# Kernel tuning notes

Measured on AMD Instinct MI355X. Metric: run time of the kernel, lower is better.

The kernel has to match this reference:

```python
import jax, jax.numpy as jnp
import numpy as np

B, N = 16, 4096

def _fps(xyz, npoint):
    # iterative farthest point sampling on one cloud [n,3] -> [npoint] int32
    n = xyz.shape[0]
    def body(carry, _):
        dist, far = carry
        d = jnp.sum((xyz - xyz[far]) ** 2, axis=-1)
        dist = jnp.minimum(dist, d)
        return (dist, jnp.argmax(dist).astype(jnp.int32)), far
    _, idx = jax.lax.scan(body, (jnp.full((n,), 1e10, jnp.float32), jnp.int32(0)), None, length=npoint)
    return idx

def _ball_query(radius, nsample, xyz, new_xyz):
    # xyz [n,3], new_xyz [S,3] -> [S,nsample] neighbor indices (first-in-index order, as in PointNet++)
    n = xyz.shape[0]
    sqr = jnp.sum((new_xyz[:, None, :] - xyz[None, :, :]) ** 2, axis=-1)  # [S,n]
    idx = jnp.where(sqr > radius * radius, n, jnp.arange(n, dtype=jnp.int32)[None, :])
    idx = jnp.sort(idx, axis=-1)[:, :nsample]
    return jnp.where(idx == n, idx[:, :1], idx)

def _gather(p, i):
    return jax.vmap(lambda pp, ii: pp[ii])(p, i)

def _mlp(x, layers):
    # shared MLP = 1x1 conv over grouped points; BN(eval) folded into (W,b)
    for W, b in layers:
        x = jax.nn.relu(jnp.einsum('bsnc,co->bsno', x, W) + b)
    return x

def _sa(xyz, feats, npoint, radius, nsample, layers):
    fps_idx = jax.vmap(lambda p: _fps(p, npoint))(xyz)            # [B,S]
    new_xyz = _gather(xyz, fps_idx)                                # [B,S,3]
    idx = jax.vmap(lambda p, q: _ball_query(radius, nsample, p, q))(xyz, new_xyz)  # [B,S,ns]
    x = _gather(xyz, idx) - new_xyz[:, :, None, :]                 # centered grouped xyz
    if feats is not None:
        x = jnp.concatenate([x, _gather(feats, idx)], axis=-1)
    x = _mlp(x, layers)
    return new_xyz, jnp.max(x, axis=2)

def _forward(points, w10, b10, w11, b11, w12, b12, w20, b20, w21, b21, w22, b22, w30, b30, w31, b31, w32, b32, lw1, lb1, lw2, lb2, fw1, fb1, fw2, fb2, pos_mean, pos_std, rot_mean, rot_std):
    l1x, l1f = _sa(points, None, 512, 0.2, 32, [(w10, b10), (w11, b11), (w12, b12)])
    l2x, l2f = _sa(l1x, l1f, 128, 0.4, 64, [(w20, b20), (w21, b21), (w22, b22)])
    # sa3: group_all
    x = jnp.concatenate([l2x, l2f], axis=-1)[:, None]              # [B,1,128,259]
    x = _mlp(x, [(w30, b30), (w31, b31), (w32, b32)])
    g = jnp.max(x, axis=2).reshape(points.shape[0], 1024)
    label = jax.nn.sigmoid(jax.nn.relu(g @ lw1 + lb1) @ lw2 + lb2)  # dropout = identity (eval)
    res = jax.nn.relu(g @ fw1 + fb1) @ fw2 + fb2
    pl = res[:, 0:3] * pos_std + pos_mean
    rl = res[:, 3:9] * rot_std + rot_mean
    pr = res[:, 9:12] * pos_std + pos_mean
    rr = res[:, 12:18] * rot_std + rot_mean
    return jnp.concatenate([label, pl, rl, pr, rr], axis=-1)       # [B,20]

def setup_inputs():
    ks = iter(jax.random.split(jax.random.key(0), 64))
    def w(shape, s=0.05):
        return jax.random.normal(next(ks), shape, jnp.float32) * s
    inp = {'points': jax.random.normal(next(ks), (B, N, 3), jnp.float32) * 0.5}
    dims = {'w10': (3, 64), 'w11': (64, 64), 'w12': (64, 128), 'w20': (131, 128), 'w21': (128, 128), 'w22': (128, 256), 'w30': (259, 256), 'w31': (256, 512), 'w32': (512, 1024), 'lw1': (1024, 256), 'lw2': (256, 2), 'fw1': (1024, 512), 'fw2': (512, 18)}
    for name, s in dims.items():
        inp[name] = w(s)
        inp[name.replace('w', 'b', 1)] = jnp.zeros((s[1],), jnp.float32)
    inp['pos_mean'] = w((3,), 0.1)
    inp['pos_std'] = jnp.abs(w((3,))) + 1.0
    inp['rot_mean'] = w((6,), 0.1)
    inp['rot_std'] = jnp.abs(w((6,))) + 1.0
    return inp

def reference(points, w10, b10, w11, b11, w12, b12, w20, b20, w21, b21, w22, b22, w30, b30, w31, b31, w32, b32, lw1, lb1, lw2, lb2, fw1, fb1, fw2, fb2, pos_mean, pos_std, rot_mean, rot_std):
    return _forward(points, w10, b10, w11, b11, w12, b12, w20, b20, w21, b21, w22, b22, w30, b30, w31, b31, w32, b32, lw1, lb1, lw2, lb2, fw1, fb1, fw2, fb2, pos_mean, pos_std, rot_mean, rot_std)
```

## Files before the change

kernel.cpp:

```cpp
#include <hip/hip_runtime.h>
#include <math.h>

#define BB 16
#define NN 4096

typedef float v2f __attribute__((ext_vector_type(2)));
typedef short bfrag8 __attribute__((ext_vector_type(8)));
typedef float fx4 __attribute__((ext_vector_type(4)));

__device__ __forceinline__ v2f pkfma(v2f a, v2f b, v2f c) {
    return __builtin_elementwise_fma(a, b, c);
}

__device__ __forceinline__ fx4 mfma16(bfrag8 a, bfrag8 b, fx4 c) {
    return __builtin_amdgcn_mfma_f32_16x16x32_bf16(a, b, c, 0, 0, 0);
}

__device__ __forceinline__ unsigned short bf16rne(float v) {
    unsigned u = __float_as_uint(v);
    return (unsigned short)((u + 0x7FFFu + ((u >> 16) & 1u)) >> 16);
}
__device__ __forceinline__ void bf16split(float v, unsigned short& h, unsigned short& l) {
    h = bf16rne(v);
    float fh = __uint_as_float((unsigned)h << 16);
    l = bf16rne(v - fh);
}

__device__ __forceinline__ float sq3(float dx, float dy, float dz) {
    return __fadd_rn(__fadd_rn(__fmul_rn(dx, dx), __fmul_rn(dy, dy)), __fmul_rn(dz, dz));
}

template<int CTRL, int RMASK>
__device__ __forceinline__ unsigned long long dpp_max_step(unsigned long long P) {
    int lo = __builtin_amdgcn_update_dpp(0, (int)(unsigned)P,        CTRL, RMASK, 0xf, true);
    int hi = __builtin_amdgcn_update_dpp(0, (int)(unsigned)(P >> 32), CTRL, RMASK, 0xf, true);
    unsigned long long o = ((unsigned long long)(unsigned)hi << 32) | (unsigned)lo;
    return (o > P) ? o : P;
}

__device__ __forceinline__ unsigned long long dpp_wave_max_u64(unsigned long long P) {
    P = dpp_max_step<0x111, 0xf>(P);
    P = dpp_max_step<0x112, 0xf>(P);
    P = dpp_max_step<0x114, 0xf>(P);
    P = dpp_max_step<0x118, 0xf>(P);
    P = dpp_max_step<0x142, 0xa>(P);
    P = dpp_max_step<0x143, 0xc>(P);
    return P;
}

__device__ __forceinline__ unsigned long long u64max(unsigned long long a, unsigned long long b) {
    return (a > b) ? a : b;
}

template<int NPTS, int NPOINT, int TPB>
__global__ __launch_bounds__(TPB) void fps_kernel(const float* __restrict__ xyz,
                                                  float* __restrict__ newxyz,
                                                  float* __restrict__ out_t,
                                                  int ts) {
    constexpr int PPT = NPTS / TPB;
    constexpr int NW  = TPB / 64;
    static_assert(NPOINT <= TPB, "far-history latch needs NPOINT <= TPB");
    __shared__ float sx[NPTS], sy[NPTS], sz[NPTS];
    __shared__ __align__(16) unsigned long long slot[2][NW];
    const int b = blockIdx.x;
    const int tid = threadIdx.x;
    const float* base = xyz + (size_t)b * NPTS * 3;
    for (int i = tid; i < NPTS; i += TPB) {
        sx[i] = base[i * 3 + 0];
        sy[i] = base[i * 3 + 1];
        sz[i] = base[i * 3 + 2];
    }
    __syncthreads();
    float px[PPT], py[PPT], pz[PPT], dist[PPT];
#pragma unroll
    for (int k = 0; k < PPT; k++) {
        int p = tid + k * TPB;
        px[k] = sx[p]; py[k] = sy[p]; pz[k] = sz[p];
        dist[k] = 1e10f;
    }
    int far = 0;
    int myfar = 0;
    const int lane = tid & 63, wid = tid >> 6;
    for (int it = 0; it < NPOINT; it++) {
        if (tid == it) myfar = far;
        float fx = sx[far], fy = sy[far], fz = sz[far];
        float bv = -1.0f; int bi = 0;
#pragma unroll
        for (int k = 0; k < PPT; k++) {
            float d = sq3(px[k] - fx, py[k] - fy, pz[k] - fz);
            float nd = fminf(dist[k], d);
            dist[k] = nd;
            if (nd > bv) { bv = nd; bi = tid + k * TPB; }
        }
        unsigned long long P = ((unsigned long long)__float_as_uint(bv) << 32)
                             | (unsigned long long)(~(unsigned)bi & 0xFFFFFFFFull);
        P = dpp_wave_max_u64(P);
        int bufi = it & 1;
        if (lane == 63) slot[bufi][wid] = P;
        __syncthreads();
        unsigned long long v[NW];
#pragma unroll
        for (int w = 0; w < NW; w++) v[w] = slot[bufi][w];
#pragma unroll
        for (int st = NW / 2; st >= 1; st >>= 1)
#pragma unroll
            for (int w = 0; w < st; w++) v[w] = u64max(v[w], v[w + st]);
        far = (int)(~(unsigned)(v[0] & 0xFFFFFFFFull));
    }
    if (tid < NPOINT) {
        float fx = sx[myfar], fy = sy[myfar], fz = sz[myfar];
        newxyz[((size_t)b * NPOINT + tid) * 3 + 0] = fx;
        newxyz[((size_t)b * NPOINT + tid) * 3 + 1] = fy;
        newxyz[((size_t)b * NPOINT + tid) * 3 + 2] = fz;
        if (out_t) {
            out_t[0 * ts + b * NPOINT + tid] = fx;
            out_t[1 * ts + b * NPOINT + tid] = fy;
            out_t[2 * ts + b * NPOINT + tid] = fz;
        }
    }
}

template<int NS>
__device__ __forceinline__ void bq_body(const float* __restrict__ pts, int n,
                                        const float* __restrict__ centers, int S,
                                        float r2, int* __restrict__ outidx,
                                        int wave, int lane) {
    int b = wave / S, s = wave % S;
    const float* c = centers + ((size_t)b * S + s) * 3;
    float cx = c[0], cy = c[1], cz = c[2];
    const float* pb = pts + (size_t)b * n * 3;
    int* out = outidx + ((size_t)b * S + s) * NS;
    int total = 0, first = -1;
    int rounds = n >> 6;
    for (int r = 0; r < rounds; r++) {
        int p = (r << 6) + lane;
        float dx = pb[p * 3 + 0] - cx, dy = pb[p * 3 + 1] - cy, dz = pb[p * 3 + 2] - cz;
        float d = sq3(dx, dy, dz);
        bool pred = (d <= r2);
        unsigned long long mask = __ballot(pred);
        if (first < 0 && mask) first = (r << 6) + (__ffsll(mask) - 1);
        if (pred) {
            int rank = total + __popcll(mask & ((1ull << lane) - 1ull));
            if (rank < NS) out[rank] = p;
        }
        total += __popcll(mask);
        if (total >= NS) break;
    }
    for (int j = total + lane; j < NS; j += 64) out[j] = first;
}

__device__ __forceinline__ void wconv_one(const float* __restrict__ W, float* __restrict__ OF,
                                          int NT, int KT, int N, int t) {
    int L = t & 63;
    int rest = t >> 6;
    int nt = rest & (NT - 1);
    int hk = rest / NT;
    int kt = hk % KT, hl = hk / KT;
    int k0 = kt * 32 + (L >> 4) * 8;
    int n  = nt * 16 + (L & 15);
    unsigned o[4];
#pragma unroll
    for (int e = 0; e < 4; e++) {
        float va = W[(size_t)(k0 + 2 * e + 0) * N + n];
        float vb = W[(size_t)(k0 + 2 * e + 1) * N + n];
        unsigned short ha, la, hb, lb;
        bf16split(va, ha, la);
        bf16split(vb, hb, lb);
        o[e] = hl ? ((unsigned)la | ((unsigned)lb << 16))
                  : ((unsigned)ha | ((unsigned)hb << 16));
    }
    ((uint4*)OF)[t] = make_uint4(o[0], o[1], o[2], o[3]);
}

__global__ __launch_bounds__(512) void bq1_fps2_kernel(const float* __restrict__ points,
                                                       const float* __restrict__ l1x,
                                                       float* __restrict__ l2x,
                                                       float* __restrict__ x3t,
                                                       int* __restrict__ idx1,
                                                       float r2a,
                                                       const float* __restrict__ w21,
                                                       const float* __restrict__ w22,
                                                       const float* __restrict__ w11s,
                                                       const float* __restrict__ w12s,
                                                       const float* __restrict__ w20s,
                                                       float* __restrict__ w21f,
                                                       float* __restrict__ w22f,
                                                       float* __restrict__ w11f,
                                                       float* __restrict__ w12f,
                                                       float* __restrict__ w20f) {
    __shared__ float sx[512], sy[512], sz[512];
    const int tid = threadIdx.x;
    const int lane = tid & 63, wid = tid >> 6;
    if (blockIdx.x < 16) {
        if (wid != 0) return;
        const int b = blockIdx.x;
        const float* base = l1x + (size_t)b * 512 * 3;
        for (int i = lane; i < 512; i += 64) {
            sx[i] = base[i * 3 + 0];
            sy[i] = base[i * 3 + 1];
            sz[i] = base[i * 3 + 2];
        }
        float px[8], py[8], pz[8], dist[8];
#pragma unroll
        for (int k = 0; k < 8; k++) {
            int p = lane + k * 64;
            px[k] = sx[p]; py[k] = sy[p]; pz[k] = sz[p];
            dist[k] = 1e10f;
        }
        int far = 0, myfar0 = 0, myfar1 = 0;
        for (int it = 0; it < 128; it++) {
            if (lane == it) myfar0 = far;
            if (lane == it - 64) myfar1 = far;
            float fx = sx[far], fy = sy[far], fz = sz[far];
            float bv = -1.0f; int bi = 0;
#pragma unroll
            for (int k = 0; k < 8; k++) {
                float d = sq3(px[k] - fx, py[k] - fy, pz[k] - fz);
                float nd = fminf(dist[k], d);
                dist[k] = nd;
                if (nd > bv) { bv = nd; bi = lane + k * 64; }
            }
            unsigned long long P = ((unsigned long long)__float_as_uint(bv) << 32)
                                 | (unsigned long long)(~(unsigned)bi & 0xFFFFFFFFull);
            P = dpp_wave_max_u64(P);
            unsigned lo = (unsigned)__builtin_amdgcn_readlane((int)(unsigned)P, 63);
            far = (int)(~lo);
        }
        {
            int s0 = lane, s1 = lane + 64;
            float a = sx[myfar0], c1 = sy[myfar0], c2 = sz[myfar0];
            l2x[((size_t)b * 128 + s0) * 3 + 0] = a;
            l2x[((size_t)b * 128 + s0) * 3 + 1] = c1;
            l2x[((size_t)b * 128 + s0) * 3 + 2] = c2;
            x3t[0 * 2048 + b * 128 + s0] = a;
            x3t[1 * 2048 + b * 128 + s0] = c1;
            x3t[2 * 2048 + b * 128 + s0] = c2;
            float d = sx[myfar1], e = sy[myfar1], f = sz[myfar1];
            l2x[((size_t)b * 128 + s1) * 3 + 0] = d;
            l2x[((size_t)b * 128 + s1) * 3 + 1] = e;
            l2x[((size_t)b * 128 + s1) * 3 + 2] = f;
            x3t[0 * 2048 + b * 128 + s1] = d;
            x3t[1 * 2048 + b * 128 + s1] = e;
            x3t[2 * 2048 + b * 128 + s1] = f;
        }
    } else if (blockIdx.x < 1040) {
        int wave = (blockIdx.x - 16) * 8 + wid;
        bq_body<32>(points, 4096, l1x, 512, r2a, idx1, wave, lane);
    } else {
        int gt = (blockIdx.x - 1040) * 512 + tid;
        if (gt < 4096)       wconv_one(w21,        w21f, 8,  4, 128, gt);
        else if (gt < 12288) wconv_one(w22,        w22f, 16, 4, 256, gt - 4096);
        else if (gt < 13312) wconv_one(w11s,       w11f, 4,  2, 64,  gt - 12288);
        else if (gt < 15360) wconv_one(w12s,       w12f, 8,  2, 128, gt - 13312);
        else                 wconv_one(w20s + 384, w20f, 8,  4, 128, gt - 15360);
    }
}

__global__ __launch_bounds__(64, 2) void sa1_bq2_kernel(const float* __restrict__ xyz, const float* __restrict__ l1x,
                                                 const int* __restrict__ idx1,
                                                 const float* __restrict__ l2x, int* __restrict__ idx2, float r2b,
                                                 const float* __restrict__ W1, const float* __restrict__ B1,
                                                 const float* __restrict__ W2f, const float* __restrict__ B2,
                                                 const float* __restrict__ W3f, const float* __restrict__ B3,
                                                 float* __restrict__ l1f) {
    __shared__ short hsh[64 * 72];
    __shared__ short hsl[64 * 72];
    int lane = threadIdx.x;
    if (blockIdx.x < 2048) {
        bq_body<64>(l1x, 512, l2x, 128, r2b, idx2, blockIdx.x, lane);
        return;
    }
    int blk = blockIdx.x - 2048;
    int b = blk >> 8;
    int ct = lane >> 5, nn = lane & 31;
    int s = ((blk & 255) << 1) | ct;
    int center = b * 512 + s;
    int c0 = b * 512 + ((blk & 255) << 1);
    int ii = idx1[center * 32 + nn];
    float px = xyz[((size_t)b * NN + ii) * 3 + 0] - l1x[(size_t)center * 3 + 0];
    float py = xyz[((size_t)b * NN + ii) * 3 + 1] - l1x[(size_t)center * 3 + 1];
    float pz = xyz[((size_t)b * NN + ii) * 3 + 2] - l1x[(size_t)center * 3 + 2];
#pragma unroll
    for (int c2 = 0; c2 < 32; c2++) {
        int ca = 2 * c2, cb = 2 * c2 + 1;
        float v0 = fmaxf(B1[ca] + px * W1[ca] + py * W1[64 + ca] + pz * W1[128 + ca], 0.0f);
        float v1 = fmaxf(B1[cb] + px * W1[cb] + py * W1[64 + cb] + pz * W1[128 + cb], 0.0f);
        unsigned short h0, l0, h1, l1;
        bf16split(v0, h0, l0);
        bf16split(v1, h1, l1);
        int base = lane * 72 + ca;
        *(unsigned*)(&hsh[base]) = (unsigned)h0 | ((unsigned)h1 << 16);
        *(unsigned*)(&hsl[base]) = (unsigned)l0 | ((unsigned)l1 << 16);
    }
    __syncthreads();
    {
        fx4 acc[4][4];
#pragma unroll
        for (int mt = 0; mt < 4; mt++)
#pragma unroll
            for (int nt = 0; nt < 4; nt++) {
                float bn = B2[nt * 16 + (lane & 15)];
                acc[mt][nt] = (fx4){bn, bn, bn, bn};
// ... 45 lines not shown
#pragma unroll
        for (int mt = 0; mt < 4; mt++)
#pragma unroll
            for (int nt = 0; nt < 4; nt++) {
                float bn = B3[(nbase + nt) * 16 + (lane & 15)];
                acc[mt][nt] = (fx4){bn, bn, bn, bn};
            }
#pragma unroll
        for (int kt = 0; kt < 2; kt++) {
            bfrag8 ah[4], al[4];
#pragma unroll
            for (int mt = 0; mt < 4; mt++) {
                int idx = (mt * 16 + (lane & 15)) * 72 + kt * 32 + (lane >> 4) * 8;
                ah[mt] = *(const bfrag8*)(&hsh[idx]);
                al[mt] = *(const bfrag8*)(&hsl[idx]);
            }
#pragma unroll
            for (int nt = 0; nt < 4; nt++) {
                bfrag8 bh = w3v[(size_t)((0 + kt) * 8 + nbase + nt) * 64 + lane];
                bfrag8 bl = w3v[(size_t)((2 + kt) * 8 + nbase + nt) * 64 + lane];
#pragma unroll
                for (int mt = 0; mt < 4; mt++) {
                    acc[mt][nt] = mfma16(ah[mt], bh, acc[mt][nt]);
                    acc[mt][nt] = mfma16(ah[mt], bl, acc[mt][nt]);
                    acc[mt][nt] = mfma16(al[mt], bh, acc[mt][nt]);
                }
            }
        }
#pragma unroll
        for (int nt = 0; nt < 4; nt++) {
            float mv0 = 0.0f, mv1 = 0.0f;
#pragma unroll
            for (int r = 0; r < 4; r++) {
                mv0 = fmaxf(mv0, fmaxf(acc[0][nt][r], acc[1][nt][r]));
                mv1 = fmaxf(mv1, fmaxf(acc[2][nt][r], acc[3][nt][r]));
            }
            mv0 = fmaxf(mv0, __shfl_xor(mv0, 16));
            mv0 = fmaxf(mv0, __shfl_xor(mv0, 32));
            mv1 = fmaxf(mv1, __shfl_xor(mv1, 16));
            mv1 = fmaxf(mv1, __shfl_xor(mv1, 32));
            int n = (nbase + nt) * 16 + (lane & 15);
            if (lane < 16)      l1f[(size_t)c0 * 128 + n] = mv0;
            else if (lane < 32) l1f[(size_t)(c0 + 1) * 128 + n] = mv1;
        }
    }
}

__global__ __launch_bounds__(256, 4) void sa2_kernel(const float* __restrict__ l1x, const float* __restrict__ l2x,
                                                  const float* __restrict__ l1f, const int* __restrict__ idx2,
                                                  const float* __restrict__ W1, const float* __restrict__ B1,
                                                  const float* __restrict__ w20f,
                                                  const float* __restrict__ w21f, const float* __restrict__ B2,
                                                  const float* __restrict__ w22f, const float* __restrict__ B3,
                                                  float* __restrict__ x3t) {
    __shared__ short hsh[64 * 136];
    __shared__ short hsl[64 * 136];
    __shared__ float sxyz[64 * 4];
    int tid = threadIdx.x;
    int w = __builtin_amdgcn_readfirstlane(tid >> 6);
    int lane = tid & 63;
    int b = blockIdx.x >> 7, s = blockIdx.x & 127;
    int center = b * 128 + s;
    int ii = idx2[center * 64 + lane];
    float cx = l2x[(size_t)center * 3 + 0], cy = l2x[(size_t)center * 3 + 1], cz = l2x[(size_t)center * 3 + 2];
    const float* pr = l1x + ((size_t)b * 512 + ii) * 3;
    float px = pr[0] - cx, py = pr[1] - cy, pz = pr[2] - cz;
    if (w == 0) {
        sxyz[lane * 4 + 0] = px;
        sxyz[lane * 4 + 1] = py;
        sxyz[lane * 4 + 2] = pz;
    }
    {
        const float4* frow = (const float4*)(l1f + ((size_t)b * 512 + ii) * 128);
#pragma unroll
        for (int j = 0; j < 8; j++) {
            float4 f = frow[w * 8 + j];
            unsigned short h0, l0, h1, l1, h2, l2, h3, l3;
            bf16split(f.x, h0, l0);
            bf16split(f.y, h1, l1);
            bf16split(f.z, h2, l2);
            bf16split(f.w, h3, l3);
            int cb = lane * 136 + w * 32 + 4 * j;
            *(unsigned*)(&hsh[cb + 0]) = (unsigned)h0 | ((unsigned)h1 << 16);
            *(unsigned*)(&hsh[cb + 2]) = (unsigned)h2 | ((unsigned)h3 << 16);
            *(unsigned*)(&hsl[cb + 0]) = (unsigned)l0 | ((unsigned)l1 << 16);
            *(unsigned*)(&hsl[cb + 2]) = (unsigned)l2 | ((unsigned)l3 << 16);
        }
    }
    __syncthreads();
    {
        fx4 acc[4][2];
        float w0n[2], w1n[2], w2n[2];
#pragma unroll
        for (int nt = 0; nt < 2; nt++) {
            int n = (2 * w + nt) * 16 + (lane & 15);
            float bn = B1[n];
            acc[0][nt] = (fx4){bn, bn, bn, bn};
            acc[1][nt] = acc[0][nt]; acc[2][nt] = acc[0][nt]; acc[3][nt] = acc[0][nt];
            w0n[nt] = W1[n]; w1n[nt] = W1[128 + n]; w2n[nt] = W1[256 + n];
        }
#pragma unroll
        for (int mt = 0; mt < 4; mt++)
#pragma unroll
            for (int r = 0; r < 4; r++) {
                int m = mt * 16 + (lane >> 4) * 4 + r;
                float mx = sxyz[m * 4 + 0], my = sxyz[m * 4 + 1], mz = sxyz[m * 4 + 2];
#pragma unroll
                for (int nt = 0; nt < 2; nt++)
                    acc[mt][nt][r] += mx * w0n[nt] + my * w1n[nt] + mz * w2n[nt];
            }
#pragma unroll
// ... 118 lines not shown
#pragma unroll
        for (int nt = 0; nt < 2; nt++) {
            float mv = 0.0f;
#pragma unroll
            for (int mt = 0; mt < 4; mt++)
#pragma unroll
                for (int r = 0; r < 4; r++)
                    mv = fmaxf(mv, acc[mt][nt][r]);
            mv = fmaxf(mv, __shfl_xor(mv, 16));
            mv = fmaxf(mv, __shfl_xor(mv, 32));
            if (lane < 16)
                x3t[(size_t)(3 + (nb + nt) * 16 + lane) * 2048 + center] = mv;
        }
    }
}

template<int K, int COUT, int CPT>
__device__ __forceinline__ void gemm1_body_bf16out(const float* __restrict__ in_t,
                                                   const float* __restrict__ W,
                                                   const float* __restrict__ bias,
                                                   unsigned short* __restrict__ oh,
                                                   unsigned short* __restrict__ ol,
                                                   int bid, int lane) {
    int rw = bid & 31, cg = bid >> 5;
    int row = rw * 64 + lane;
    int cbase = cg * CPT;
    v2f acc[CPT / 2];
    const v2f* bv = (const v2f*)(bias + cbase);
#pragma unroll
    for (int j = 0; j < CPT / 2; j++) acc[j] = bv[j];
    for (int k = 0; k < K; k++) {
        float xk = in_t[(size_t)k * 2048 + row];
        v2f xk2 = {xk, xk};
        const v2f* wr = (const v2f*)(W + (size_t)k * COUT + cbase);
#pragma unroll
        for (int j = 0; j < CPT / 2; j++) acc[j] = pkfma(xk2, wr[j], acc[j]);
    }
    unsigned ho[4], lo[4];
#pragma unroll
    for (int j = 0; j < CPT / 2; j++) {
        float va = fmaxf(acc[j].x, 0.0f);
        float vb = fmaxf(acc[j].y, 0.0f);
        unsigned short ha, la, hb, lb;
        bf16split(va, ha, la);
        bf16split(vb, hb, lb);
        ho[j] = (unsigned)ha | ((unsigned)hb << 16);
        lo[j] = (unsigned)la | ((unsigned)lb << 16);
    }
    size_t idx = ((size_t)row * COUT + cbase) >> 3;
    ((uint4*)oh)[idx] = make_uint4(ho[0], ho[1], ho[2], ho[3]);
    ((uint4*)ol)[idx] = make_uint4(lo[0], lo[1], lo[2], lo[3]);
}

__global__ __launch_bounds__(64, 4) void gemm1_zerog_kernel(const float* __restrict__ in_t,
                                                            const float* __restrict__ W,
                                                            const float* __restrict__ bias,
                                                            unsigned short* __restrict__ h1h,
                                                            unsigned short* __restrict__ h1l,
                                                            float* __restrict__ g,
                                                            const float* __restrict__ w31,
                                                            const float* __restrict__ w32,
                                                            float* __restrict__ w31f,
                                                            float* __restrict__ w32f) {
    if (blockIdx.x < 1024) {
        gemm1_body_bf16out<259, 256, 8>(in_t, W, bias, h1h, h1l, blockIdx.x, threadIdx.x);
    } else if (blockIdx.x < 1280) {
        g[(blockIdx.x - 1024) * 64 + threadIdx.x] = 0.0f;
    } else {
        int gt = (blockIdx.x - 1280) * 64 + threadIdx.x;
        if (gt < 32768) wconv_one(w31, w31f, 32, 8,  512,  gt);
        else            wconv_one(w32, w32f, 64, 16, 1024, gt - 32768);
    }
}

template<int K, int NT_TOT, bool MAXOUT>
__global__ __launch_bounds__(64, 4) void gemm_mfma_kernel(const unsigned short* __restrict__ Ah,
                                                          const unsigned short* __restrict__ Al,
                                                          const float* __restrict__ Wf,
                                                          const float* __restrict__ bias,
                                                          unsigned short* __restrict__ Oh,
                                                          unsigned short* __restrict__ Ol,
                                                          float* __restrict__ g) {
    constexpr int KT = K / 32;
    constexpr int NCOL = NT_TOT * 16;
    int lane = threadIdx.x;
    int mtile = blockIdx.x & 31, bn = blockIdx.x >> 5;
    int mbase = mtile * 64;
    int nb4 = bn * 4;
    const bfrag8* wv = (const bfrag8*)Wf;
    fx4 acc[4][4];
#pragma unroll
    for (int mt = 0; mt < 4; mt++)
#pragma unroll
        for (int j = 0; j < 4; j++) {
            float bnv = bias[(nb4 + j) * 16 + (lane & 15)];
            acc[mt][j] = (fx4){bnv, bnv, bnv, bnv};
        }
#pragma unroll 1
    for (int kt = 0; kt < KT; kt++) {
        bfrag8 ah[4], al[4];
#pragma unroll
        for (int mt = 0; mt < 4; mt++) {
            size_t off = (size_t)(mbase + mt * 16 + (lane & 15)) * K + kt * 32 + (lane >> 4) * 8;
            ah[mt] = *(const bfrag8*)(Ah + off);
            al[mt] = *(const bfrag8*)(Al + off);
        }
#pragma unroll
        for (int j = 0; j < 4; j++) {
            bfrag8 bh = wv[(size_t)((0 * KT + kt) * NT_TOT + nb4 + j) * 64 + lane];
            bfrag8 bl = wv[(size_t)((1 * KT + kt) * NT_TOT + nb4 + j) * 64 + lane];
#pragma unroll
            for (int mt = 0; mt < 4; mt++) {
                acc[mt][j] = mfma16(ah[mt], bh, acc[mt][j]);
                acc[mt][j] = mfma16(ah[mt], bl, acc[mt][j]);
                acc[mt][j] = mfma16(al[mt], bh, acc[mt][j]);
            }
        }
    }
    if (MAXOUT) {
        int b = mbase >> 7;
#pragma unroll
        for (int j = 0; j < 4; j++) {
            float mv = 0.0f;
#pragma unroll
            for (int mt = 0; mt < 4; mt++)
#pragma unroll
                for (int r = 0; r < 4; r++)
                    mv = fmaxf(mv, acc[mt][j][r]);
            mv = fmaxf(mv, __shfl_xor(mv, 16));
            mv = fmaxf(mv, __shfl_xor(mv, 32));
            if (lane < 16)
                atomicMax((int*)(g + (size_t)b * 1024 + (nb4 + j) * 16 + lane), __float_as_int(mv));
        }
    } else {
#pragma unroll
        for (int mt = 0; mt < 4; mt++)
#pragma unroll
            for (int j = 0; j < 4; j++)
#pragma unroll
                for (int r = 0; r < 4; r++) {
                    float v = fmaxf(acc[mt][j][r], 0.0f);
                    int m = mbase + mt * 16 + (lane >> 4) * 4 + r;
                    int n = (nb4 + j) * 16 + (lane & 15);
                    unsigned short hb, lb;
                    bf16split(v, hb, lb);
                    Oh[(size_t)m * NCOL + n] = hb;
                    Ol[(size_t)m * NCOL + n] = lb;
                }
    }
}

__global__ __launch_bounds__(512) void head_kernel(const float* __restrict__ g,
                                                   const float* __restrict__ lw1, const float* __restrict__ lb1,
                                                   const float* __restrict__ lw2, const float* __restrict__ lb2,
                                                   const float* __restrict__ fw1, const float* __restrict__ fb1,
                                                   const float* __restrict__ fw2, const float* __restrict__ fb2,
                                                   const float* __restrict__ pm, const float* __restrict__ ps,
                                                   const float* __restrict__ rm, const float* __restrict__ rs,
                                                   float* __restrict__ out) {
    __shared__ float gl[1024], a1[256], f1[512];
    int b = blockIdx.x, t = threadIdx.x;
    for (int i = t; i < 1024; i += 512) gl[i] = g[b * 1024 + i];
    __syncthreads();
    {
        float acc = fb1[t];
        for (int k = 0; k < 1024; k++) acc += gl[k] * fw1[k * 512 + t];
        f1[t] = fmaxf(acc, 0.0f);
    }
    if (t < 256) {
        float acc = lb1[t];
        for (int k = 0; k < 1024; k++) acc += gl[k] * lw1[k * 256 + t];
        a1[t] = fmaxf(acc, 0.0f);
    }
    __syncthreads();
    if (t < 2) {
        float z = lb2[t];
        for (int k = 0; k < 256; k++) z += a1[k] * lw2[k * 2 + t];
        out[b * 20 + t] = 1.0f / (1.0f + expf(-z));
    } else if (t < 20) {
        int i = t - 2;
        float z = fb2[i];
        for (int k = 0; k < 512; k++) z += f1[k] * fw2[k * 18 + i];
        float sc, mn;
        if (i < 3)       { sc = ps[i];      mn = pm[i]; }
        else if (i < 9)  { sc = rs[i - 3];  mn = rm[i - 3]; }
        else if (i < 12) { sc = ps[i - 9];  mn = pm[i - 9]; }
        else             { sc = rs[i - 12]; mn = rm[i - 12]; }
        out[b * 20 + t] = z * sc + mn;
    }
}

static inline size_t align256(size_t x) { return (x + 255) & ~(size_t)255; }

extern "C" void kernel_launch(void* const* d_in, const int* in_sizes, int n_in,
                              void* d_out, int out_size, void* d_ws, size_t ws_size,
                              hipStream_t stream) {
    const float* points = (const float*)d_in[0];
    const float* w10 = (const float*)d_in[1];  const float* b10 = (const float*)d_in[2];
    const float* w11 = (const float*)d_in[3];  const float* b11 = (const float*)d_in[4];
    const float* w12 = (const float*)d_in[5];  const float* b12 = (const float*)d_in[6];
    const float* w20 = (const float*)d_in[7];  const float* b20 = (const float*)d_in[8];
    const float* w21 = (const float*)d_in[9];  const float* b21 = (const float*)d_in[10];
    const float* w22 = (const float*)d_in[11]; const float* b22 = (const float*)d_in[12];
    const float* w30 = (const float*)d_in[13]; const float* b30 = (const float*)d_in[14];
    const float* w31 = (const float*)d_in[15]; const float* b31 = (const float*)d_in[16];
    const float* w32 = (const float*)d_in[17]; const float* b32 = (const float*)d_in[18];
    const float* lw1 = (const float*)d_in[19]; const float* lb1 = (const float*)d_in[20];
    const float* lw2 = (const float*)d_in[21]; const float* lb2 = (const float*)d_in[22];
    const float* fw1 = (const float*)d_in[23]; const float* fb1 = (const float*)d_in[24];
    const float* fw2 = (const float*)d_in[25]; const float* fb2 = (const float*)d_in[26];
    const float* pm  = (const float*)d_in[27]; const float* ps  = (const float*)d_in[28];
    const float* rm  = (const float*)d_in[29]; const float* rs  = (const float*)d_in[30];
    float* out = (float*)d_out;

    char* p = (char*)d_ws;
    float* l1x  = (float*)p; p += align256((size_t)BB * 512 * 3 * 4);
    int*   idx1 = (int*)p;   p += align256((size_t)BB * 512 * 32 * 4);
    float* l1f  = (float*)p; p += align256((size_t)BB * 512 * 128 * 4);
    float* l2x  = (float*)p; p += align256((size_t)BB * 128 * 3 * 4);
    int*   idx2 = (int*)p;   p += align256((size_t)BB * 128 * 64 * 4);
    float* x3t  = (float*)p; p += align256((size_t)259 * 2048 * 4);
    float* h1t  = (float*)p; p += align256((size_t)256 * 2048 * 4);
    float* h2t  = (float*)p; p += align256((size_t)512 * 2048 * 4);
    float* g    = (float*)p; p += align256((size_t)BB * 1024 * 4);
    float* w21f = h1t;
    float* w22f = h1t + (size_t)16384;
    float* w11f = h1t + (size_t)49152;
    float* w12f = h1t + (size_t)53248;
    float* w20f = h1t + (size_t)61440;
    unsigned short* h1h = (unsigned short*)h1t;
    unsigned short* h1l = h1h + (size_t)2048 * 256;
    unsigned short* h2h = (unsigned short*)h2t;
    unsigned short* h2l = h2h + (size_t)2048 * 512;
    float* w31f = l1f;
    float* w32f = l1f + (size_t)131072;

    const float R2A = (float)(0.2 * 0.2);
    const float R2B = (float)(0.4 * 0.4);

    fps_kernel<4096, 512, 512><<<BB, 512, 0, stream>>>(points, l1x, (float*)nullptr, 0);
    bq1_fps2_kernel<<<1078, 512, 0, stream>>>(points, l1x, l2x, x3t, idx1, R2A,
                                              w21, w22, w11, w12, w20,
                                              w21f, w22f, w11f, w12f, w20f);
    sa1_bq2_kernel<<<6144, 64, 0, stream>>>(points, l1x, idx1, l2x, idx2, R2B,
                                            w10, b10, w11f, b11, w12f, b12, l1f);
    sa2_kernel<<<2048, 256, 0, stream>>>(l1x, l2x, l1f, idx2, w20, b20,
                                         w20f, w21f, b21, w22f, b22, x3t);
    gemm1_zerog_kernel<<<3840, 64, 0, stream>>>(x3t, w30, b30, h1h, h1l, g, w31, w32, w31f, w32f);
    gemm_mfma_kernel<256, 32, false><<<256, 64, 0, stream>>>(h1h, h1l, w31f, b31, h2h, h2l, (float*)nullptr);
    gemm_mfma_kernel<512, 64, true><<<512, 64, 0, stream>>>(h2h, h2l, w32f, b32,
                                                            (unsigned short*)nullptr, (unsigned short*)nullptr, g);
    head_kernel<<<BB, 512, 0, stream>>>(g, lw1, lb1, lw2, lb2, fw1, fb1, fw2, fb2, pm, ps, rm, rs, out);
}
```

Baseline: 764.0 us.

## Fuse tail GEMMs and head into one persistent kernel with grid barriers

Four tail launches become one persistent tail_kernel of 256 blocks: the first-layer GEMM with zeroing of g and weight conversion, the two MFMA GEMMs, and the head MLP. Stages are separated by a software grid barrier built on global atomics, and sa2_kernel resets the barrier counters. The head work is also spread across 192 waves instead of 16 blocks, with intermediate activations staged in reused workspace. The aim is to cut launch gaps and inter-kernel drain. In exchange it relies on all 256 blocks being co-resident and pays for spin-wait barriers.

After: 1.137 ms. 1.49x slower.

```diff
diff --git a/kernel.cpp b/kernel.cpp
--- a/kernel.cpp
+++ b/kernel.cpp
@@ -3,6 +3,7 @@
 
 #define BB 16
 #define NN 4096
+#define TAIL_BLOCKS 256
 
 typedef float v2f __attribute__((ext_vector_type(2)));
 typedef short bfrag8 __attribute__((ext_vector_type(8)));
@@ -50,6 +51,24 @@
 
 __device__ __forceinline__ unsigned long long u64max(unsigned long long a, unsigned long long b) {
     return (a > b) ? a : b;
+}
+
+__device__ __forceinline__ void grid_barrier(unsigned* cnt, unsigned* gen) {
+    __syncthreads();
+    if (threadIdx.x == 0) {
+        unsigned g0 = __hip_atomic_load(gen, __ATOMIC_ACQUIRE, __HIP_MEMORY_SCOPE_AGENT);
+        __threadfence();
+        unsigned a = __hip_atomic_fetch_add(cnt, 1u, __ATOMIC_ACQ_REL, __HIP_MEMORY_SCOPE_AGENT);
+        if (a == TAIL_BLOCKS - 1) {
+            __hip_atomic_store(cnt, 0u, __ATOMIC_RELAXED, __HIP_MEMORY_SCOPE_AGENT);
+            __hip_atomic_fetch_add(gen, 1u, __ATOMIC_ACQ_REL, __HIP_MEMORY_SCOPE_AGENT);
+        } else {
+            while (__hip_atomic_load(gen, __ATOMIC_ACQUIRE, __HIP_MEMORY_SCOPE_AGENT) == g0)
+                __builtin_amdgcn_s_sleep(8);
+        }
+    }
+    __syncthreads();
+    __threadfence();
 }
 
 template<int NPTS, int NPOINT, int TPB>
@@ -399,11 +418,13 @@
                                                   const float* __restrict__ w20f,
                                                   const float* __restrict__ w21f, const float* __restrict__ B2,
                                                   const float* __restrict__ w22f, const float* __restrict__ B3,
-                                                  float* __restrict__ x3t) {
+                                                  float* __restrict__ x3t,
+                                                  unsigned* __restrict__ bar) {
     __shared__ short hsh[64 * 136];
     __shared__ short hsl[64 * 136];
     __shared__ float sxyz[64 * 4];
     int tid = threadIdx.x;
+    if (blockIdx.x == 0 && tid == 0) { bar[0] = 0u; bar[1] = 0u; }
     int w = __builtin_amdgcn_readfirstlane(tid >> 6);
     int lane = tid & 63;
     int b = blockIdx.x >> 7, s = blockIdx.x & 127;
@@ -628,39 +649,18 @@
     ((uint4*)ol)[idx] = make_uint4(lo[0], lo[1], lo[2], lo[3]);
 }
 
-__global__ __launch_bounds__(64, 4) void gemm1_zerog_kernel(const float* __restrict__ in_t,
-                                                            const float* __restrict__ W,
-                                                            const float* __restrict__ bias,
-                                                            unsigned short* __restrict__ h1h,
-                                                            unsigned short* __restrict__ h1l,
-                                                            float* __restrict__ g,
-                                                            const float* __restrict__ w31,
-                                                            const float* __restrict__ w32,
-                                                            float* __restrict__ w31f,
-                                                            float* __restrict__ w32f) {
-    if (blockIdx.x < 1024) {
-        gemm1_body_bf16out<259, 256, 8>(in_t, W, bias, h1h, h1l, blockIdx.x, threadIdx.x);
-    } else if (blockIdx.x < 1280) {
-        g[(blockIdx.x - 1024) * 64 + threadIdx.x] = 0.0f;
-    } else {
-        int gt = (blockIdx.x - 1280) * 64 + threadIdx.x;
-        if (gt < 32768) wconv_one(w31, w31f, 32, 8,  512,  gt);
-        else            wconv_one(w32, w32f, 64, 16, 1024, gt - 32768);
-    }
-}
-
 template<int K, int NT_TOT, bool MAXOUT>
-__global__ __launch_bounds__(64, 4) void gemm_mfma_kernel(const unsigned short* __restrict__ Ah,
-                                                          const unsigned short* __restrict__ Al,
-                                                          const float* __restrict__ Wf,
-                                                          const float* __restrict__ bias,
-                                                          unsigned short* __restrict__ Oh,
-                                                          unsigned short* __restrict__ Ol,
-                                                          float* __restrict__ g) {
+__device__ __forceinline__ void gemm_mfma_body(const unsigned short* __restrict__ Ah,
+                                               const unsigned short* __restrict__ Al,
+                                               const float* __restrict__ Wf,
+                                               const float* __restrict__ bias,
+                                               unsigned short* __restrict__ Oh,
+                                               unsigned short* __restrict__ Ol,
+                                               float* __restrict__ g,
+                                               int bid, int lane) {
     constexpr int KT = K / 32;
     constexpr int NCOL = NT_TOT * 16;
-    int lane = threadIdx.x;
-    int mtile = blockIdx.x & 31, bn = blockIdx.x >> 5;
+    int mtile = bid & 31, bn = bid >> 5;
     int mbase = mtile * 64;
     int nb4 = bn * 4;
     const bfrag8* wv = (const bfrag8*)Wf;
@@ -726,43 +726,72 @@
     }
 }
 
-__global__ __launch_bounds__(512) void head_kernel(const float* __restrict__ g,
+__global__ __launch_bounds__(256) void tail_kernel(const float* __restrict__ x3t,
+                                                   const float* __restrict__ w30, const float* __restrict__ b30,
+                                                   unsigned short* __restrict__ h1h, unsigned short* __restrict__ h1l,
+                                                   float* __restrict__ g,
+                                                   const float* __restrict__ w31, const float* __restrict__ w32,
+                                                   float* __restrict__ w31f, float* __restrict__ w32f,
+                                                   const float* __restrict__ b31,
+                                                   unsigned short* __restrict__ h2h, unsigned short* __restrict__ h2l,
+                                                   const float* __restrict__ b32,
+                                                   const float* __restrict__ fw1, const float* __restrict__ fb1,
                                                    const float* __restrict__ lw1, const float* __restrict__ lb1,
+                                                   const float* __restrict__ fw2, const float* __restrict__ fb2,
                                                    const float* __restrict__ lw2, const float* __restrict__ lb2,
-                                                   const float* __restrict__ fw1, const float* __restrict__ fb1,
-                                                   const float* __restrict__ fw2, const float* __restrict__ fb2,
                                                    const float* __restrict__ pm, const float* __restrict__ ps,
                                                    const float* __restrict__ rm, const float* __restrict__ rs,
-                                                   float* __restrict__ out) {
-    __shared__ float gl[1024], a1[256], f1[512];
-    int b = blockIdx.x, t = threadIdx.x;
-    for (int i = t; i < 1024; i += 512) gl[i] = g[b * 1024 + i];
-    __syncthreads();
-    {
+                                                   float* __restrict__ out,
+                                                   unsigned* __restrict__ bar,
+                                                   float* __restrict__ f1g, float* __restrict__ a1g) {
+    int tid = threadIdx.x;
+    int lane = tid & 63, wid = tid >> 6;
+    int vw = blockIdx.x * 4 + wid;
+    gemm1_body_bf16out<259, 256, 8>(x3t, w30, b30, h1h, h1l, vw, lane);
+    if (vw < 256) g[vw * 64 + lane] = 0.0f;
+    for (int it = vw * 64 + lane; it < 163840; it += 65536) {
+        if (it < 32768) wconv_one(w31, w31f, 32, 8, 512, it);
+        else            wconv_one(w32, w32f, 64, 16, 1024, it - 32768);
+    }
+    grid_barrier(bar, bar + 1);
+    if (vw < 256)
+        gemm_mfma_body<256, 32, false>(h1h, h1l, w31f, b31, h2h, h2l, (float*)nullptr, vw, lane);
+    grid_barrier(bar, bar + 1);
+    if (vw < 512)
+        gemm_mfma_body<512, 64, true>(h2h, h2l, w32f, b32,
+                                      (unsigned short*)nullptr, (unsigned short*)nullptr, g, vw, lane);
+    grid_barrier(bar, bar + 1);
+    if (vw < 128) {
+        int item = vw * 64 + lane;
+        int b = item >> 9, t = item & 511;
         float acc = fb1[t];
-        for (int k = 0; k < 1024; k++) acc += gl[k] * fw1[k * 512 + t];
-        f1[t] = fmaxf(acc, 0.0f);
-    }
-    if (t < 256) {
+        for (int k = 0; k < 1024; k++) acc += g[b * 1024 + k] * fw1[k * 512 + t];
+        f1g[b * 512 + t] = fmaxf(acc, 0.0f);
+    } else if (vw < 192) {
+        int item = (vw - 128) * 64 + lane;
+        int b = item >> 8, t = item & 255;
         float acc = lb1[t];
-        for (int k = 0; k < 1024; k++) acc += gl[k] * lw1[k * 256 + t];
-        a1[t] = fmaxf(acc, 0.0f);
-    }
-    __syncthreads();
-    if (t < 2) {
-        float z = lb2[t];
-        for (int k = 0; k < 256; k++) z += a1[k] * lw2[k * 2 + t];
-        out[b * 20 + t] = 1.0f / (1.0f + expf(-z));
-    } else if (t < 20) {
-        int i = t - 2;
-        float z = fb2[i];
-        for (int k = 0; k < 512; k++) z += f1[k] * fw2[k * 18 + i];
-        float sc, mn;
-        if (i < 3)       { sc = ps[i];      mn = pm[i]; }
-        else if (i < 9)  { sc = rs[i - 3];  mn = rm[i - 3]; }
-        else if (i < 12) { sc = ps[i - 9];  mn = pm[i - 9]; }
-        else             { sc = rs[i - 12]; mn = rm[i - 12]; }
-        out[b * 20 + t] = z * sc + mn;
+        for (int k = 0; k < 1024; k++) acc += g[b * 1024 + k] * lw1[k * 256 + t];
+        a1g[b * 256 + t] = fmaxf(acc, 0.0f);
+    }
+    grid_barrier(bar, bar + 1);
+    if (vw < 16) {
+        int b = vw, t = lane;
+        if (t < 2) {
+            float z = lb2[t];
+            for (int k = 0; k < 256; k++) z += a1g[b * 256 + k] * lw2[k * 2 + t];
+            out[b * 20 + t] = 1.0f / (1.0f + expf(-z));
+        } else if (t < 20) {
+            int i = t - 2;
+            float z = fb2[i];
+            for (int k = 0; k < 512; k++) z += f1g[b * 512 + k] * fw2[k * 18 + i];
+            float sc, mn;
+            if (i < 3)       { sc = ps[i];      mn = pm[i]; }
+            else if (i < 9)  { sc = rs[i - 3];  mn = rm[i - 3]; }
+            else if (i < 12) { sc = ps[i - 9];  mn = pm[i - 9]; }
+            else             { sc = rs[i - 12]; mn = rm[i - 12]; }
+            out[b * 20 + t] = z * sc + mn;
+        }
     }
 }
 
@@ -810,6 +839,9 @@
     unsigned short* h2l = h2h + (size_t)2048 * 512;
     float* w31f = l1f;
     float* w32f = l1f + (size_t)131072;
+    float* f1g = x3t;
+    float* a1g = x3t + (size_t)8192;
+    unsigned* bar = (unsigned*)idx1;
 
     const float R2A = (float)(0.2 * 0.2);
     const float R2B = (float)(0.4 * 0.4);
@@ -821,10 +853,9 @@
     sa1_bq2_kernel<<<6144, 64, 0, stream>>>(points, l1x, idx1, l2x, idx2, R2B,
                                             w10, b10, w11f, b11, w12f, b12, l1f);
     sa2_kernel<<<2048, 256, 0, stream>>>(l1x, l2x, l1f, idx2, w20, b20,
-                                         w20f, w21f, b21, w22f, b22, x3t);
-    gemm1_zerog_kernel<<<3840, 64, 0, stream>>>(x3t, w30, b30, h1h, h1l, g, w31, w32, w31f, w32f);
-    gemm_mfma_kernel<256, 32, false><<<256, 64, 0, stream>>>(h1h, h1l, w31f, b31, h2h, h2l, (float*)nullptr);
-    gemm_mfma_kernel<512, 64, true><<<512, 64, 0, stream>>>(h2h, h2l, w32f, b32,
-                                                            (unsigned short*)nullptr, (unsigned short*)nullptr, g);
-    head_kernel<<<BB, 512, 0, stream>>>(g, lw1, lb1, lw2, lb2, fw1, fb1, fw2, fb2, pm, ps, rm, rs, out);
-}
+                                         w20f, w21f, b21, w22f, b22, x3t, bar);
+    tail_kernel<<<TAIL_BLOCKS, 256, 0, stream>>>(x3t, w30, b30, h1h, h1l, g,
+                                                 w31, w32, w31f, w32f, b31, h2h, h2l, b32,
+                                                 fw1, fb1, lw1, lb1, fw2, fb2, lw2, lb2,
+                                                 pm, ps, rm, rs, out, bar, f1g, a1g);
+}
```

## Move second-level FPS into first FPS kernel via per-batch spin-wait flags

Applied to the files above, without the earlier changes.

The 128-point FPS on the l1 centroids moves out of the ball-query kernel and into extra blocks of the first FPS launch. Each of these blocks spin-waits on a per-batch global flag that the matching first-level FPS block sets with a release store after writing its centroids. This takes the serial second FPS off the critical path of the ball-query kernel and overlaps it with the tail of the first FPS. The cost is a reliance on all 32 blocks being co-resident to avoid deadlock. It also reuses the g buffer as flag storage, which must not already hold the magic value and must be zeroed later before use.

Result: no change. 774.8 us (+1.4%).

```diff
diff --git a/kernel.cpp b/kernel.cpp
--- a/kernel.cpp
+++ b/kernel.cpp
@@ -3,6 +3,7 @@
 
 #define BB 16
 #define NN 4096
+#define FPS2_MAGIC 0xF1A60001u
 
 typedef float v2f __attribute__((ext_vector_type(2)));
 typedef short bfrag8 __attribute__((ext_vector_type(8)));
@@ -55,15 +56,74 @@
 template<int NPTS, int NPOINT, int TPB>
 __global__ __launch_bounds__(TPB) void fps_kernel(const float* __restrict__ xyz,
                                                   float* __restrict__ newxyz,
-                                                  float* __restrict__ out_t,
-                                                  int ts) {
+                                                  float* __restrict__ l2x,
+                                                  float* __restrict__ x3t,
+                                                  unsigned* __restrict__ gflag) {
     constexpr int PPT = NPTS / TPB;
     constexpr int NW  = TPB / 64;
     static_assert(NPOINT <= TPB, "far-history latch needs NPOINT <= TPB");
     __shared__ float sx[NPTS], sy[NPTS], sz[NPTS];
     __shared__ __align__(16) unsigned long long slot[2][NW];
+    const int tid = threadIdx.x;
+    const int lane = tid & 63, wid = tid >> 6;
+    if (blockIdx.x >= 16) {
+        if (wid != 0) return;
+        const int b = blockIdx.x - 16;
+        while (__hip_atomic_load(&gflag[b], __ATOMIC_ACQUIRE, __HIP_MEMORY_SCOPE_AGENT) != FPS2_MAGIC)
+            __builtin_amdgcn_s_sleep(32);
+        __threadfence();
+        const float* base = newxyz + (size_t)b * 512 * 3;
+        for (int i = lane; i < 512; i += 64) {
+            sx[i] = base[i * 3 + 0];
+            sy[i] = base[i * 3 + 1];
+            sz[i] = base[i * 3 + 2];
+        }
+        float px[8], py[8], pz[8], dist[8];
+#pragma unroll
+        for (int k = 0; k < 8; k++) {
+            int p = lane + k * 64;
+            px[k] = sx[p]; py[k] = sy[p]; pz[k] = sz[p];
+            dist[k] = 1e10f;
+        }
+        int far = 0, myfar0 = 0, myfar1 = 0;
+        for (int it = 0; it < 128; it++) {
+            if (lane == it) myfar0 = far;
+            if (lane == it - 64) myfar1 = far;
+            float fx = sx[far], fy = sy[far], fz = sz[far];
+            float bv = -1.0f; int bi = 0;
+#pragma unroll
+            for (int k = 0; k < 8; k++) {
+                float d = sq3(px[k] - fx, py[k] - fy, pz[k] - fz);
+                float nd = fminf(dist[k], d);
+                dist[k] = nd;
+                if (nd > bv) { bv = nd; bi = lane + k * 64; }
+            }
+            unsigned long long P = ((unsigned long long)__float_as_uint(bv) << 32)
+                                 | (unsigned long long)(~(unsigned)bi & 0xFFFFFFFFull);
+            P = dpp_wave_max_u64(P);
+            unsigned lo = (unsigned)__builtin_amdgcn_readlane((int)(unsigned)P, 63);
+            far = (int)(~lo);
+        }
+        {
+            int s0 = lane, s1 = lane + 64;
+            float a = sx[myfar0], c1 = sy[myfar0], c2 = sz[myfar0];
+            l2x[((size_t)b * 128 + s0) * 3 + 0] = a;
+            l2x[((size_t)b * 128 + s0) * 3 + 1] = c1;
+            l2x[((size_t)b * 128 + s0) * 3 + 2] = c2;
+            x3t[0 * 2048 + b * 128 + s0] = a;
+            x3t[1 * 2048 + b * 128 + s0] = c1;
+            x3t[2 * 2048 + b * 128 + s0] = c2;
+            float d = sx[myfar1], e = sy[myfar1], f = sz[myfar1];
+            l2x[((size_t)b * 128 + s1) * 3 + 0] = d;
+            l2x[((size_t)b * 128 + s1) * 3 + 1] = e;
+            l2x[((size_t)b * 128 + s1) * 3 + 2] = f;
+            x3t[0 * 2048 + b * 128 + s1] = d;
+            x3t[1 * 2048 + b * 128 + s1] = e;
+            x3t[2 * 2048 + b * 128 + s1] = f;
+        }
+        return;
+    }
     const int b = blockIdx.x;
-    const int tid = threadIdx.x;
     const float* base = xyz + (size_t)b * NPTS * 3;
     for (int i = tid; i < NPTS; i += TPB) {
         sx[i] = base[i * 3 + 0];
@@ -80,7 +140,6 @@
     }
     int far = 0;
     int myfar = 0;
-    const int lane = tid & 63, wid = tid >> 6;
     for (int it = 0; it < NPOINT; it++) {
         if (tid == it) myfar = far;
         float fx = sx[far], fy = sy[far], fz = sz[far];
@@ -112,11 +171,11 @@
         newxyz[((size_t)b * NPOINT + tid) * 3 + 0] = fx;
         newxyz[((size_t)b * NPOINT + tid) * 3 + 1] = fy;
         newxyz[((size_t)b * NPOINT + tid) * 3 + 2] = fz;
-        if (out_t) {
-            out_t[0 * ts + b * NPOINT + tid] = fx;
-            out_t[1 * ts + b * NPOINT + tid] = fy;
-            out_t[2 * ts + b * NPOINT + tid] = fz;
-        }
+    }
+    __syncthreads();
+    if (tid == 0) {
+        __threadfence();
+        __hip_atomic_store(&gflag[b], FPS2_MAGIC, __ATOMIC_RELEASE, __HIP_MEMORY_SCOPE_AGENT);
     }
 }
 
@@ -172,82 +231,27 @@
     ((uint4*)OF)[t] = make_uint4(o[0], o[1], o[2], o[3]);
 }
 
-__global__ __launch_bounds__(512) void bq1_fps2_kernel(const float* __restrict__ points,
-                                                       const float* __restrict__ l1x,
-                                                       float* __restrict__ l2x,
-                                                       float* __restrict__ x3t,
-                                                       int* __restrict__ idx1,
-                                                       float r2a,
-                                                       const float* __restrict__ w21,
-                                                       const float* __restrict__ w22,
-                                                       const float* __restrict__ w11s,
-                                                       const float* __restrict__ w12s,
-                                                       const float* __restrict__ w20s,
-                                                       float* __restrict__ w21f,
-                                                       float* __restrict__ w22f,
-                                                       float* __restrict__ w11f,
-                                                       float* __restrict__ w12f,
-                                                       float* __restrict__ w20f) {
-    __shared__ float sx[512], sy[512], sz[512];
+__global__ __launch_bounds__(512) void bq1_kernel(const float* __restrict__ points,
+                                                  const float* __restrict__ l1x,
+                                                  int* __restrict__ idx1,
+                                                  float r2a,
+                                                  const float* __restrict__ w21,
+                                                  const float* __restrict__ w22,
+                                                  const float* __restrict__ w11s,
+                                                  const float* __restrict__ w12s,
+                                                  const float* __restrict__ w20s,
+                                                  float* __restrict__ w21f,
+                                                  float* __restrict__ w22f,
+                                                  float* __restrict__ w11f,
+                                                  float* __restrict__ w12f,
+                                                  float* __restrict__ w20f) {
     const int tid = threadIdx.x;
     const int lane = tid & 63, wid = tid >> 6;
-    if (blockIdx.x < 16) {
-        if (wid != 0) return;
-        const int b = blockIdx.x;
-        const float* base = l1x + (size_t)b * 512 * 3;
-        for (int i = lane; i < 512; i += 64) {
-            sx[i] = base[i * 3 + 0];
-            sy[i] = base[i * 3 + 1];
-            sz[i] = base[i * 3 + 2];
-        }
-        float px[8], py[8], pz[8], dist[8];
-#pragma unroll
-        for (int k = 0; k < 8; k++) {
-            int p = lane + k * 64;
-            px[k] = sx[p]; py[k] = sy[p]; pz[k] = sz[p];
-            dist[k] = 1e10f;
-        }
-        int far = 0, myfar0 = 0, myfar1 = 0;
-        for (int it = 0; it < 128; it++) {
-            if (lane == it) myfar0 = far;
-            if (lane == it - 64) myfar1 = far;
-            float fx = sx[far], fy = sy[far], fz = sz[far];
-            float bv = -1.0f; int bi = 0;
-#pragma unroll
-            for (int k = 0; k < 8; k++) {
-                float d = sq3(px[k] - fx, py[k] - fy, pz[k] - fz);
-                float nd = fminf(dist[k], d);
-                dist[k] = nd;
-                if (nd > bv) { bv = nd; bi = lane + k * 64; }
-            }
-            unsigned long long P = ((unsigned long long)__float_as_uint(bv) << 32)
-                                 | (unsigned long long)(~(unsigned)bi & 0xFFFFFFFFull);
-            P = dpp_wave_max_u64(P);
-            unsigned lo = (unsigned)__builtin_amdgcn_readlane((int)(unsigned)P, 63);
-            far = (int)(~lo);
-        }
-        {
-            int s0 = lane, s1 = lane + 64;
-            float a = sx[myfar0], c1 = sy[myfar0], c2 = sz[myfar0];
-            l2x[((size_t)b * 128 + s0) * 3 + 0] = a;
-            l2x[((size_t)b * 128 + s0) * 3 + 1] = c1;
-            l2x[((size_t)b * 128 + s0) * 3 + 2] = c2;
-            x3t[0 * 2048 + b * 128 + s0] = a;
-            x3t[1 * 2048 + b * 128 + s0] = c1;
-            x3t[2 * 2048 + b * 128 + s0] = c2;
-            float d = sx[myfar1], e = sy[myfar1], f = sz[myfar1];
-            l2x[((size_t)b * 128 + s1) * 3 + 0] = d;
-            l2x[((size_t)b * 128 + s1) * 3 + 1] = e;
-            l2x[((size_t)b * 128 + s1) * 3 + 2] = f;
-            x3t[0 * 2048 + b * 128 + s1] = d;
-            x3t[1 * 2048 + b * 128 + s1] = e;
-            x3t[2 * 2048 + b * 128 + s1] = f;
-        }
-    } else if (blockIdx.x < 1040) {
-        int wave = (blockIdx.x - 16) * 8 + wid;
+    if (blockIdx.x < 1024) {
+        int wave = blockIdx.x * 8 + wid;
         bq_body<32>(points, 4096, l1x, 512, r2a, idx1, wave, lane);
     } else {
-        int gt = (blockIdx.x - 1040) * 512 + tid;
+        int gt = (blockIdx.x - 1024) * 512 + tid;
         if (gt < 4096)       wconv_one(w21,        w21f, 8,  4, 128, gt);
         else if (gt < 12288) wconv_one(w22,        w22f, 16, 4, 256, gt - 4096);
         else if (gt < 13312) wconv_one(w11s,       w11f, 4,  2, 64,  gt - 12288);
@@ -814,10 +818,10 @@
     const float R2A = (float)(0.2 * 0.2);
     const float R2B = (float)(0.4 * 0.4);
 
-    fps_kernel<4096, 512, 512><<<BB, 512, 0, stream>>>(points, l1x, (float*)nullptr, 0);
-    bq1_fps2_kernel<<<1078, 512, 0, stream>>>(points, l1x, l2x, x3t, idx1, R2A,
-                                              w21, w22, w11, w12, w20,
-                                              w21f, w22f, w11f, w12f, w20f);
+    fps_kernel<4096, 512, 512><<<32, 512, 0, stream>>>(points, l1x, l2x, x3t, (unsigned*)g);
+    bq1_kernel<<<1062, 512, 0, stream>>>(points, l1x, idx1, R2A,
+                                         w21, w22, w11, w12, w20,
+                                         w21f, w22f, w11f, w12f, w20f);
     sa1_bq2_kernel<<<6144, 64, 0, stream>>>(points, l1x, idx1, l2x, idx2, R2B,
                                             w10, b10, w11f, b11, w12f, b12, l1f);
     sa2_kernel<<<2048, 256, 0, stream>>>(l1x, l2x, l1f, idx2, w20, b20,
```

## Fuse final MFMA GEMM with head MLP using last-block atomic counter

Applied to the files above, without the earlier changes.

Folds the last 512-tile MFMA GEMM (with max-reduce into g) and the head MLP into one kernel of 64 blocks with 8 waves each. Each wave handles one virtual tile. A per-batch atomic counter, zeroed in the gemm1 kernel, lets the last finishing block per batch run the head layers. This removes one kernel launch and its dependency gap. In exchange, the GEMM tiles now run as 8-wave blocks with 512-thread launch bounds, which may reduce occupancy or raise register pressure, and it adds fence and atomic overhead.

Result: slower. 782.2 us (+2.4%).

```diff
diff --git a/kernel.cpp b/kernel.cpp
--- a/kernel.cpp
+++ b/kernel.cpp
@@ -637,11 +637,13 @@
                                                             const float* __restrict__ w31,
                                                             const float* __restrict__ w32,
                                                             float* __restrict__ w31f,
-                                                            float* __restrict__ w32f) {
+                                                            float* __restrict__ w32f,
+                                                            unsigned* __restrict__ cnt) {
     if (blockIdx.x < 1024) {
         gemm1_body_bf16out<259, 256, 8>(in_t, W, bias, h1h, h1l, blockIdx.x, threadIdx.x);
     } else if (blockIdx.x < 1280) {
         g[(blockIdx.x - 1024) * 64 + threadIdx.x] = 0.0f;
+        if (blockIdx.x == 1024 && threadIdx.x < 16) cnt[threadIdx.x] = 0u;
     } else {
         int gt = (blockIdx.x - 1280) * 64 + threadIdx.x;
         if (gt < 32768) wconv_one(w31, w31f, 32, 8,  512,  gt);
@@ -650,17 +652,17 @@
 }
 
 template<int K, int NT_TOT, bool MAXOUT>
-__global__ __launch_bounds__(64, 4) void gemm_mfma_kernel(const unsigned short* __restrict__ Ah,
-                                                          const unsigned short* __restrict__ Al,
-                                                          const float* __restrict__ Wf,
-                                                          const float* __restrict__ bias,
-                                                          unsigned short* __restrict__ Oh,
-                                                          unsigned short* __restrict__ Ol,
-                                                          float* __restrict__ g) {
+__device__ __forceinline__ void gemm_mfma_body(const unsigned short* __restrict__ Ah,
+                                               const unsigned short* __restrict__ Al,
+                                               const float* __restrict__ Wf,
+                                               const float* __restrict__ bias,
+                                               unsigned short* __restrict__ Oh,
+                                               unsigned short* __restrict__ Ol,
+                                               float* __restrict__ g,
+                                               int bid, int lane) {
     constexpr int KT = K / 32;
     constexpr int NCOL = NT_TOT * 16;
-    int lane = threadIdx.x;
-    int mtile = blockIdx.x & 31, bn = blockIdx.x >> 5;
+    int mtile = bid & 31, bn = bid >> 5;
     int mbase = mtile * 64;
     int nb4 = bn * 4;
     const bfrag8* wv = (const bfrag8*)Wf;
@@ -726,35 +728,66 @@
     }
 }
 
-__global__ __launch_bounds__(512) void head_kernel(const float* __restrict__ g,
-                                                   const float* __restrict__ lw1, const float* __restrict__ lb1,
-                                                   const float* __restrict__ lw2, const float* __restrict__ lb2,
-                                                   const float* __restrict__ fw1, const float* __restrict__ fb1,
-                                                   const float* __restrict__ fw2, const float* __restrict__ fb2,
-                                                   const float* __restrict__ pm, const float* __restrict__ ps,
-                                                   const float* __restrict__ rm, const float* __restrict__ rs,
-                                                   float* __restrict__ out) {
+template<int K, int NT_TOT, bool MAXOUT>
+__global__ __launch_bounds__(64, 4) void gemm_mfma_kernel(const unsigned short* __restrict__ Ah,
+                                                          const unsigned short* __restrict__ Al,
+                                                          const float* __restrict__ Wf,
+                                                          const float* __restrict__ bias,
+                                                          unsigned short* __restrict__ Oh,
+                                                          unsigned short* __restrict__ Ol,
+                                                          float* __restrict__ g) {
+    gemm_mfma_body<K, NT_TOT, MAXOUT>(Ah, Al, Wf, bias, Oh, Ol, g, blockIdx.x, threadIdx.x);
+}
+
+__global__ __launch_bounds__(512) void gemm3_head_kernel(const unsigned short* __restrict__ Ah,
+                                                         const unsigned short* __restrict__ Al,
+                                                         const float* __restrict__ Wf,
+                                                         const float* __restrict__ bias,
+                                                         float* __restrict__ g,
+                                                         unsigned* __restrict__ cnt,
+                                                         const float* __restrict__ lw1, const float* __restrict__ lb1,
+                                                         const float* __restrict__ lw2, const float* __restrict__ lb2,
+                                                         const float* __restrict__ fw1, const float* __restrict__ fb1,
+                                                         const float* __restrict__ fw2, const float* __restrict__ fb2,
+                                                         const float* __restrict__ pm, const float* __restrict__ ps,
+                                                         const float* __restrict__ rm, const float* __restrict__ rs,
+                                                         float* __restrict__ out) {
     __shared__ float gl[1024], a1[256], f1[512];
-    int b = blockIdx.x, t = threadIdx.x;
-    for (int i = t; i < 1024; i += 512) gl[i] = g[b * 1024 + i];
+    __shared__ int lastflag;
+    int tid = threadIdx.x;
+    int lane = tid & 63, wid = tid >> 6;
+    int vtile = wid * 64 + blockIdx.x;
+    gemm_mfma_body<512, 64, true>(Ah, Al, Wf, bias,
+                                  (unsigned short*)nullptr, (unsigned short*)nullptr, g, vtile, lane);
+    int b = (blockIdx.x & 31) >> 1;
+    __syncthreads();
+    if (tid == 0) {
+        __threadfence();
+        unsigned r = __hip_atomic_fetch_add(&cnt[b], 1u, __ATOMIC_ACQ_REL, __HIP_MEMORY_SCOPE_AGENT);
+        lastflag = (r == 3u) ? 1 : 0;
+    }
+    __syncthreads();
+    if (!lastflag) return;
+    for (int i = tid; i < 1024; i += 512)
+        gl[i] = __hip_atomic_load(g + (size_t)b * 1024 + i, __ATOMIC_RELAXED, __HIP_MEMORY_SCOPE_AGENT);
     __syncthreads();
     {
-        float acc = fb1[t];
-        for (int k = 0; k < 1024; k++) acc += gl[k] * fw1[k * 512 + t];
-        f1[t] = fmaxf(acc, 0.0f);
-    }
-    if (t < 256) {
-        float acc = lb1[t];
-        for (int k = 0; k < 1024; k++) acc += gl[k] * lw1[k * 256 + t];
-        a1[t] = fmaxf(acc, 0.0f);
+        float acc = fb1[tid];
+        for (int k = 0; k < 1024; k++) acc += gl[k] * fw1[k * 512 + tid];
+        f1[tid] = fmaxf(acc, 0.0f);
+    }
+    if (tid < 256) {
+        float acc = lb1[tid];
+        for (int k = 0; k < 1024; k++) acc += gl[k] * lw1[k * 256 + tid];
+        a1[tid] = fmaxf(acc, 0.0f);
     }
     __syncthreads();
-    if (t < 2) {
-        float z = lb2[t];
-        for (int k = 0; k < 256; k++) z += a1[k] * lw2[k * 2 + t];
-        out[b * 20 + t] = 1.0f / (1.0f + expf(-z));
-    } else if (t < 20) {
-        int i = t - 2;
+    if (tid < 2) {
+        float z = lb2[tid];
+        for (int k = 0; k < 256; k++) z += a1[k] * lw2[k * 2 + tid];
+        out[b * 20 + tid] = 1.0f / (1.0f + expf(-z));
+    } else if (tid < 20) {
+        int i = tid - 2;
         float z = fb2[i];
         for (int k = 0; k < 512; k++) z += f1[k] * fw2[k * 18 + i];
         float sc, mn;
@@ -762,7 +795,7 @@
         else if (i < 9)  { sc = rs[i - 3];  mn = rm[i - 3]; }
         else if (i < 12) { sc = ps[i - 9];  mn = pm[i - 9]; }
         else             { sc = rs[i - 12]; mn = rm[i - 12]; }
-        out[b * 20 + t] = z * sc + mn;
+        out[b * 20 + tid] = z * sc + mn;
     }
 }
 
@@ -810,6 +843,7 @@
     unsigned short* h2l = h2h + (size_t)2048 * 512;
     float* w31f = l1f;
     float* w32f = l1f + (size_t)131072;
+    unsigned* cnt = (unsigned*)idx1;
 
     const float R2A = (float)(0.2 * 0.2);
     const float R2B = (float)(0.4 * 0.4);
@@ -822,9 +856,9 @@
                                             w10, b10, w11f, b11, w12f, b12, l1f);
     sa2_kernel<<<2048, 256, 0, stream>>>(l1x, l2x, l1f, idx2, w20, b20,
                                          w20f, w21f, b21, w22f, b22, x3t);
-    gemm1_zerog_kernel<<<3840, 64, 0, stream>>>(x3t, w30, b30, h1h, h1l, g, w31, w32, w31f, w32f);
+    gemm1_zerog_kernel<<<3840, 64, 0, stream>>>(x3t, w30, b30, h1h, h1l, g, w31, w32, w31f, w32f, cnt);
     gemm_mfma_kernel<256, 32, false><<<256, 64, 0, stream>>>(h1h, h1l, w31f, b31, h2h, h2l, (float*)nullptr);
-    gemm_mfma_kernel<512, 64, true><<<512, 64, 0, stream>>>(h2h, h2l, w32f, b32,
-                                                            (unsigned short*)nullptr, (unsigned short*)nullptr, g);
-    head_kernel<<<BB, 512, 0, stream>>>(g, lw1, lb1, lw2, lb2, fw1, fb1, fw2, fb2, pm, ps, rm, rs, out);
-}
+    gemm3_head_kernel<<<64, 512, 0, stream>>>(h2h, h2l, w32f, b32, g, cnt,
+                                              lw1, lb1, lw2, lb2, fw1, fb1, fw2, fb2,
+                                              pm, ps, rm, rs, out);
+}
```
